# Kernel tuning notes

Hardware: AMD Instinct MI355X
Metric: run time of the kernel (lower is better)

The kernel has to match this reference:

```python
import jax, jax.numpy as jnp
import numpy as np

P = 7          # window size
HEADS = 8
DIM_HEAD = 32
INNER = HEADS * DIM_HEAD  # 256
DIM_IN = 256
DIM_OUT = 256
SCALE = DIM_HEAD ** -0.5


def _rel_index(p):
    i = np.array([[x, y] for x in range(p) for y in range(p)])  # (p*p, 2)
    d = i[None, :, :] - i[:, None, :]                            # (p*p, p*p, 2)
    return jnp.asarray(d + p - 1, dtype=jnp.int32)


def setup_inputs() -> dict:
    key = jax.random.key(0)
    ks = jax.random.split(key, 6)
    x = jax.random.normal(ks[0], (16, DIM_IN, 112, 112), dtype=jnp.float32)
    Wq = jax.random.normal(ks[1], (INNER, DIM_IN), dtype=jnp.float32) * 0.02
    Wkv = jax.random.normal(ks[2], (2 * INNER, DIM_IN), dtype=jnp.float32) * 0.02
    Wo = jax.random.normal(ks[3], (DIM_OUT, INNER), dtype=jnp.float32) * 0.02
    bo = jax.random.normal(ks[4], (DIM_OUT,), dtype=jnp.float32) * 0.02
    pos_embedding = jax.random.normal(ks[5], (2 * P - 1, 2 * P - 1), dtype=jnp.float32) * 0.02
    rel_index = _rel_index(P)
    return {"x": x, "Wq": Wq, "Wkv": Wkv, "Wo": Wo, "bo": bo,
            "pos_embedding": pos_embedding, "rel_index": rel_index}


def _local_attention(x, Wq, Wkv, Wo, bo, pos_embedding, rel_index):
    b, c, h, w = x.shape
    n1, n2 = h // P, w // P
    n = P * P
    # relative position bias (p^2, p^2)
    bias = pos_embedding[rel_index[:, :, 0], rel_index[:, :, 1]]
    # window partition: (b, c, n1, P, n2, P) -> (b*n1*n2, c, P*P)
    xw = x.reshape(b, c, n1, P, n2, P).transpose(0, 2, 4, 1, 3, 5)
    xw = xw.reshape(b * n1 * n2, c, n)
    # 1x1 conv projections as channel GEMMs
    q = jnp.einsum('oc,bcn->bon', Wq, xw)       # (B', INNER, n)
    kv = jnp.einsum('oc,bcn->bon', Wkv, xw)     # (B', 2*INNER, n)
    k, v = kv[:, :INNER], kv[:, INNER:]

    def to_heads(t):  # (B', H*d, n) -> (B', H, n, d)
        Bp = t.shape[0]
        return t.reshape(Bp, HEADS, DIM_HEAD, n).transpose(0, 1, 3, 2)

    q, k, v = to_heads(q), to_heads(k), to_heads(v)
    dots = jnp.einsum('bhid,bhjd->bhij', q, k) * SCALE + bias
    attn = jax.nn.softmax(dots, axis=-1)
    out = jnp.einsum('bhij,bhjd->bhid', attn, v)          # (B', H, n, d)
    out = out.transpose(0, 1, 3, 2).reshape(-1, INNER, n)  # (B', H*d, n)
    out = jnp.einsum('oc,bcn->bon', Wo, out) + bo[None, :, None]
    # window merge back to (b, c_out, h, w)
    out = out.reshape(b, n1, n2, DIM_OUT, P, P).transpose(0, 3, 1, 4, 2, 5)
    out = out.reshape(b, DIM_OUT, h, w)
    return out, attn


def reference(x, Wq, Wkv, Wo, bo, pos_embedding, rel_index):
    return _local_attention(x, Wq, Wkv, Wo, bo, pos_embedding, rel_index)
```

## Files before the change

### kernel.cpp

```cpp
#include <hip/hip_runtime.h>
#include <hip/hip_bf16.h>

typedef __bf16 bf16x8 __attribute__((ext_vector_type(8)));
typedef __bf16 bf16x4 __attribute__((ext_vector_type(4)));
typedef float  f32x4  __attribute__((ext_vector_type(4)));
typedef float  f32x16 __attribute__((ext_vector_type(16)));

#define NPOS 49
#define NHEADS 8
#define SCALE_F 0.17677669529663687f

#define SLICE_B   16896
#define QK_ROW_B  264
#define VS_OFF    8192
#define VS_ROW_B  136
#define XWT_PITCH 264
#define AOT_PITCH 264
#define BIAS_OFF  67584
#define BO_OFF    77188
#define LDS_BYTES 78212

static __device__ __forceinline__ f32x16 zero16() {
  f32x16 z;
#pragma unroll
  for (int i = 0; i < 16; ++i) z[i] = 0.f;
  return z;
}

__global__ void prep_kernel(const float* __restrict__ Wq, const float* __restrict__ Wkv,
                            const float* __restrict__ Wo, const float* __restrict__ pos,
                            const int* __restrict__ rel, __bf16* __restrict__ wqkv,
                            __bf16* __restrict__ wo, float* __restrict__ bias) {
  int idx = blockIdx.x * 256 + threadIdx.x;
  if (idx < 256 * 256) wqkv[idx] = (__bf16)Wq[idx];
  if (idx < 512 * 256) wqkv[256 * 256 + idx] = (__bf16)Wkv[idx];
  if (idx < 256 * 256) wo[idx] = (__bf16)Wo[idx];
  if (idx < 49 * 49) bias[idx] = pos[rel[idx * 2] * 13 + rel[idx * 2 + 1]];
}

template <int MODE>
__global__ __launch_bounds__(256, 2) void attn_kernel(
    const float* __restrict__ x, const __bf16* __restrict__ wqkv,
    const __bf16* __restrict__ wo, const float* __restrict__ bias_g,
    const float* __restrict__ bo_g, float* __restrict__ outg,
    float* __restrict__ attng, __bf16* __restrict__ aoT_g) {
  extern __shared__ char smem[];
  __bf16* xwT = (__bf16*)smem;
  __bf16* aoT = (__bf16*)smem;
  float* bias_s = (float*)(smem + BIAS_OFF);
  float* bo_s   = (float*)(smem + BO_OFF);

  const int tid = threadIdx.x;
  const int bid = blockIdx.x;
  const int work = (bid & 7) * 512 + (bid >> 3);
  const int b  = work >> 8;
  const int i1 = (work >> 4) & 15;
  const int i2 = work & 15;
  const int r0 = i1 * 7, c0 = i2 * 7;
  const int wave = tid >> 6, lane = tid & 63;
  const int l31 = lane & 31, g2 = lane >> 5;
  const int c16 = lane & 15, g4 = lane >> 4;
  char* slice = smem + wave * SLICE_B;

  {
    const int n = tid & 63, cb = tid >> 6;
    const int np = (n < NPOS) ? n : 0;
    const float zf = (n < NPOS) ? 1.f : 0.f;
    const int pr = np / 7, pc = np - pr * 7;
    const float* xg = x + (size_t)b * 256 * 12544 + (size_t)(r0 + pr) * 112 + (c0 + pc);
    float tmp[64];
#pragma unroll
    for (int it = 0; it < 64; ++it)
      tmp[it] = xg[(size_t)(it * 4 + cb) * 12544];
#pragma unroll
    for (int it = 0; it < 64; ++it)
      xwT[n * XWT_PITCH + it * 4 + cb] = (__bf16)(tmp[it] * zf);
    const float4* bg4 = (const float4*)bias_g;
    for (int i = tid; i < 600; i += 256) ((float4*)bias_s)[i] = bg4[i];
    if (tid == 0) bias_s[2400] = bias_g[2400];
    if constexpr (MODE == 0) bo_s[tid] = bo_g[tid];
  }
  __syncthreads();

  bf16x8 Bf0[16], Bf1[16];
  {
    const __bf16* Bp = xwT + l31 * XWT_PITCH + g2 * 8;
#pragma unroll
    for (int ks = 0; ks < 16; ++ks) {
      Bf0[ks] = *(const bf16x8*)(Bp + ks * 16);
      Bf1[ks] = *(const bf16x8*)(Bp + 32 * XWT_PITCH + ks * 16);
    }
  }
  __syncthreads();

  char* vsb = slice + VS_OFF;
  {
    const __bf16* Ap0 = wqkv + (size_t)(512 + 64 * wave + l31) * 256 + g2 * 8;
    const __bf16* Ap1 = Ap0 + 32 * 256;
    f32x16 a00 = zero16(), a01 = zero16(), a10 = zero16(), a11 = zero16();
    __builtin_amdgcn_s_setprio(1);
#pragma unroll
    for (int ks = 0; ks < 16; ++ks) {
      bf16x8 A0 = *(const bf16x8*)(Ap0 + ks * 16);
      bf16x8 A1 = *(const bf16x8*)(Ap1 + ks * 16);
      a00 = __builtin_amdgcn_mfma_f32_32x32x16_bf16(A0, Bf0[ks], a00, 0, 0, 0);
      a01 = __builtin_amdgcn_mfma_f32_32x32x16_bf16(A0, Bf1[ks], a01, 0, 0, 0);
      a10 = __builtin_amdgcn_mfma_f32_32x32x16_bf16(A1, Bf0[ks], a10, 0, 0, 0);
      a11 = __builtin_amdgcn_mfma_f32_32x32x16_bf16(A1, Bf1[ks], a11, 0, 0, 0);
    }
    __builtin_amdgcn_s_setprio(0);
#pragma unroll
    for (int rg = 0; rg < 16; ++rg) {
      const int dd = (rg & 3) + 8 * (rg >> 2) + 4 * g2;
      *(__bf16*)(vsb + dd * VS_ROW_B + l31 * 2)              = (__bf16)a00[rg];
      *(__bf16*)(vsb + dd * VS_ROW_B + 64 + l31 * 2)         = (__bf16)a01[rg];
      *(__bf16*)(vsb + (32 + dd) * VS_ROW_B + l31 * 2)       = (__bf16)a10[rg];
      *(__bf16*)(vsb + (32 + dd) * VS_ROW_B + 64 + l31 * 2)  = (__bf16)a11[rg];
    }
  }
  bf16x8 vf[2][2][2];
#pragma unroll
  for (int hh = 0; hh < 2; ++hh)
#pragma unroll
    for (int nt = 0; nt < 2; ++nt)
#pragma unroll
      for (int ks = 0; ks < 2; ++ks)
        vf[hh][nt][ks] = *(const bf16x8*)(vsb + (hh * 32 + nt * 16 + c16) * VS_ROW_B + ks * 64 + g4 * 16);
  asm volatile("s_waitcnt lgkmcnt(0)" ::: "memory");
  __builtin_amdgcn_sched_barrier(0x20);

#pragma unroll
  for (int qk = 0; qk < 2; ++qk) {
    const int rowbase = qk * 256 + 64 * wave;
    const int koff = qk * 64;
    const __bf16* Ap0 = wqkv + (size_t)(rowbase + l31) * 256 + g2 * 8;
    const __bf16* Ap1 = Ap0 + 32 * 256;
    f32x16 a00 = zero16(), a01 = zero16(), a10 = zero16(), a11 = zero16();
    __builtin_amdgcn_s_setprio(1);
#pragma unroll
    for (int ks = 0; ks < 16; ++ks) {
      bf16x8 A0 = *(const bf16x8*)(Ap0 + ks * 16);
      bf16x8 A1 = *(const bf16x8*)(Ap1 + ks * 16);
      a00 = __builtin_amdgcn_mfma_f32_32x32x16_bf16(A0, Bf0[ks], a00, 0, 0, 0);
      a01 = __builtin_amdgcn_mfma_f32_32x32x16_bf16(A0, Bf1[ks], a01, 0, 0, 0);
      a10 = __builtin_amdgcn_mfma_f32_32x32x16_bf16(A1, Bf0[ks], a10, 0, 0, 0);
      a11 = __builtin_amdgcn_mfma_f32_32x32x16_bf16(A1, Bf1[ks], a11, 0, 0, 0);
    }
    __builtin_amdgcn_s_setprio(0);
#define STORE_QK(ACC, P_, NT)                                                  \
    {                                                                          \
      const int n_ = (NT) * 32 + l31;                                          \
      _Pragma("unroll") for (int rb = 0; rb < 4; ++rb) {                       \
        const int ddb = koff + (P_) * 32 + rb * 8 + g2 * 4;                    \
        bf16x4 v4;                                                             \
        v4[0] = (__bf16)ACC[rb * 4 + 0]; v4[1] = (__bf16)ACC[rb * 4 + 1];      \
        v4[2] = (__bf16)ACC[rb * 4 + 2]; v4[3] = (__bf16)ACC[rb * 4 + 3];      \
        *(bf16x4*)(slice + n_ * QK_ROW_B + ddb * 2) = v4;                      \
      }                                                                        \
    }
    STORE_QK(a00, 0, 0)
    STORE_QK(a01, 0, 1)
    STORE_QK(a10, 1, 0)
    STORE_QK(a11, 1, 1)
  }
  bf16x8 qf[2][4], kf[2][4];
#pragma unroll
  for (int hh = 0; hh < 2; ++hh)
#pragma unroll
    for (int t = 0; t < 4; ++t) {
      qf[hh][t] = *(const bf16x8*)(slice + (t * 16 + c16) * QK_ROW_B + hh * 64 + g4 * 16);
      kf[hh][t] = *(const bf16x8*)(slice + (t * 16 + c16) * QK_ROW_B + 128 + hh * 64 + g4 * 16);
    }
  asm volatile("s_waitcnt lgkmcnt(0)" ::: "memory");
  __builtin_amdgcn_sched_barrier(0x20);

  f32x4 pacc[2][4][2];
  char* Pb0 = slice;
  char* Pb1 = slice + 8192;
  {
    const f32x4 z4 = {0.f, 0.f, 0.f, 0.f};
    f32x4 dacc[2][4][4];
    __builtin_amdgcn_s_setprio(1);
#pragma unroll
    for (int hh = 0; hh < 2; ++hh)
#pragma unroll
      for (int mt = 0; mt < 4; ++mt)
#pragma unroll
        for (int nt = 0; nt < 4; ++nt)
          dacc[hh][mt][nt] = __builtin_amdgcn_mfma_f32_16x16x32_bf16(qf[hh][mt], kf[hh][nt], z4, 0, 0, 0);
    __builtin_amdgcn_s_setprio(0);

    const int h0 = wave * 2;
#pragma unroll
    for (int mt = 0; mt < 4; ++mt) {
#pragma unroll
      for (int r = 0; r < 4; ++r) {
        const int i = mt * 16 + g4 * 4 + r;
        float p0[4], p1[4], s0 = 0.f, s1 = 0.f;
#pragma unroll
        for (int nt = 0; nt < 4; ++nt) {
          const int j = nt * 16 + c16;
          float v0 = dacc[0][mt][nt][r] * SCALE_F;
          float v1 = dacc[1][mt][nt][r] * SCALE_F;
          if (j < NPOS) {
            if (i < NPOS) { const float bb = bias_s[i * 49 + j]; v0 += bb; v1 += bb; }
          } else {
            v0 = -1e30f; v1 = -1e30f;
          }
          p0[nt] = __expf(v0); s0 += p0[nt];
          p1[nt] = __expf(v1); s1 += p1[nt];
        }
        s0 += __shfl_xor(s0, 1); s1 += __shfl_xor(s1, 1);
        s0 += __shfl_xor(s0, 2); s1 += __shfl_xor(s1, 2);
        s0 += __shfl_xor(s0, 4); s1 += __shfl_xor(s1, 4);
        s0 += __shfl_xor(s0, 8); s1 += __shfl_xor(s1, 8);
        const float inv0 = 1.f / s0, inv1 = 1.f / s1;
        if (i < NPOS) {
          float* ap0 = attng + ((size_t)(work * NHEADS + h0) * 49 + i) * 49;
          float* ap1 = ap0 + 49 * 49;
#pragma unroll
          for (int nt = 0; nt < 4; ++nt) {
            const int j = nt * 16 + c16;
            if (j < NPOS) { ap0[j] = p0[nt] * inv0; ap1[j] = p1[nt] * inv1; }
          }
        }
#pragma unroll
        for (int nt = 0; nt < 4; ++nt) {
          const int j = nt * 16 + c16;
          *(__bf16*)(Pb0 + i * 128 + 16 * ((j >> 3) ^ (i & 7)) + 2 * (j & 7)) = (__bf16)(p0[nt] * inv0);
          *(__bf16*)(Pb1 + i * 128 + 16 * ((j >> 3) ^ (i & 7)) + 2 * (j & 7)) = (__bf16)(p1[nt] * inv1);
        }
      }
    }

    __builtin_amdgcn_s_setprio(1);
#pragma unroll
    for (int hh = 0; hh < 2; ++hh) {
      char* Pb = hh ? Pb1 : Pb0;
#pragma unroll
      for (int mt = 0; mt < 4; ++mt) {
        const int i = mt * 16 + c16;
        bf16x8 pa0 = *(const bf16x8*)(Pb + i * 128 + 16 * ((0 + g4) ^ (i & 7)));
        bf16x8 pa1 = *(const bf16x8*)(Pb + i * 128 + 16 * ((4 + g4) ^ (i & 7)));
#pragma unroll
        for (int nt = 0; nt < 2; ++nt) {
          f32x4 acc = {0.f, 0.f, 0.f, 0.f};
          acc = __builtin_amdgcn_mfma_f32_16x16x32_bf16(pa0, vf[hh][nt][0], acc, 0, 0, 0);
          acc = __builtin_amdgcn_mfma_f32_16x16x32_bf16(pa1, vf[hh][nt][1], acc, 0, 0, 0);
          pacc[hh][mt][nt] = acc;
        }
      }
    }
    __builtin_amdgcn_s_setprio(0);
  }

  if constexpr (MODE == 1) {
    __bf16* ag = aoT_g + (size_t)work * 12544;
#pragma unroll
    for (int hh = 0; hh < 2; ++hh) {
      const int h = wave * 2 + hh;
#pragma unroll
      for (int mt = 0; mt < 4; ++mt)
#pragma unroll
        for (int e = 0; e < 4; ++e) {
          const int pos = mt * 16 + g4 * 4 + e;
          if (pos < NPOS) {
            ag[pos * 256 + h * 32 + c16]      = (__bf16)pacc[hh][mt][0][e];
            ag[pos * 256 + h * 32 + 16 + c16] = (__bf16)pacc[hh][mt][1][e];
          }
        }
    }
  } else {
    __syncthreads();
#pragma unroll
    for (int hh = 0; hh < 2; ++hh) {
      const int h = wave * 2 + hh;
#pragma unroll
      for (int mt = 0; mt < 4; ++mt)
#pragma unroll
        for (int nt = 0; nt < 2; ++nt)
#pragma unroll
          for (int e = 0; e < 4; ++e) {
            const int i = mt * 16 + g4 * 4 + e;
            const int cc = h * 32 + nt * 16 + c16;
            aoT[i * AOT_PITCH + cc] = (__bf16)pacc[hh][mt][nt][e];
          }
    }
    __syncthreads();
    {
      bf16x8 Cf0[16], Cf1[16];
      const __bf16* Bp = aoT + l31 * AOT_PITCH + g2 * 8;
#pragma unroll
      for (int ks = 0; ks < 16; ++ks) {
        Cf0[ks] = *(const bf16x8*)(Bp + ks * 16);
        Cf1[ks] = *(const bf16x8*)(Bp + 32 * AOT_PITCH + ks * 16);
      }
      const __bf16* Ap0 = wo + (size_t)(wave * 64 + l31) * 256 + g2 * 8;
      const __bf16* Ap1 = Ap0 + 32 * 256;
      f32x16 a00 = zero16(), a01 = zero16(), a10 = zero16(), a11 = zero16();
      __builtin_amdgcn_s_setprio(1);
#pragma unroll
      for (int ks = 0; ks < 16; ++ks) {
        bf16x8 A0 = *(const bf16x8*)(Ap0 + ks * 16);
        bf16x8 A1 = *(const bf16x8*)(Ap1 + ks * 16);
        a00 = __builtin_amdgcn_mfma_f32_32x32x16_bf16(A0, Cf0[ks], a00, 0, 0, 0);
        a01 = __builtin_amdgcn_mfma_f32_32x32x16_bf16(A0, Cf1[ks], a01, 0, 0, 0);
        a10 = __builtin_amdgcn_mfma_f32_32x32x16_bf16(A1, Cf0[ks], a10, 0, 0, 0);
        a11 = __builtin_amdgcn_mfma_f32_32x32x16_bf16(A1, Cf1[ks], a11, 0, 0, 0);
      }
      __builtin_amdgcn_s_setprio(0);
      float* og = outg + (size_t)b * 256 * 12544;
#define STORE_OUT(ACC, MT, NT)                                                    \
      {                                                                           \
        const int n_ = (NT) * 32 + l31;                                           \
        if (n_ < NPOS) {                                                          \
          const int pr_ = n_ / 7, pc_ = n_ - pr_ * 7;                             \
          float* orow = og + (size_t)(r0 + pr_) * 112 + (c0 + pc_);               \
          _Pragma("unroll") for (int rg = 0; rg < 16; ++rg) {                     \
            const int o2 = wave * 64 + (MT) * 32 + (rg & 3) + 8 * (rg >> 2) + 4 * g2; \
            orow[(size_t)o2 * 12544] = ACC[rg] + bo_s[o2];                        \
          }                                                                       \
        }                                                                         \
      }
      STORE_OUT(a00, 0, 0)
      STORE_OUT(a01, 0, 1)
      STORE_OUT(a10, 1, 0)
      STORE_OUT(a11, 1, 1)
    }
  }
}

__global__ __launch_bounds__(256, 2) void oproj_kernel(
    const __bf16* __restrict__ aoT_g, const __bf16* __restrict__ wo,
    const float* __restrict__ bo_g, float* __restrict__ outg) {
  __shared__ __bf16 aoB[112 * 264];
  __shared__ float bo_s[256];
  const int tid = threadIdx.x;
  const int bid = blockIdx.x;
  const int work = (bid & 7) * 224 + (bid >> 3);
  const int pr = work % 7;
  const int g  = work / 7;
  const int i1 = g & 15, b = g >> 4;
  const int wave = tid >> 6, lane = tid & 63;
  const int c16 = lane & 15, g4 = lane >> 4;

  {
    const int rr = tid >> 5, coff = (tid & 31) * 8;
#pragma unroll
    for (int it = 0; it < 14; ++it) {
      const int gr = it * 8 + rr;
      const int i2 = gr / 7, pc = gr - i2 * 7;
      const size_t src = ((size_t)((b * 256 + i1 * 16 + i2) * 49 + pr * 7 + pc)) * 256 + coff;
      *(bf16x8*)(aoB + gr * 264 + coff) = *(const bf16x8*)(aoT_g + src);
    }
    bo_s[tid] = bo_g[tid];
  }
  __syncthreads();

  const int oc0 = wave * 64;
  f32x4 acc[4][7];
#pragma unroll
  for (int mt = 0; mt < 4; ++mt)
#pragma unroll
    for (int nt = 0; nt < 7; ++nt) acc[mt][nt] = f32x4{0.f, 0.f, 0.f, 0.f};
#pragma unroll
  for (int kk = 0; kk < 8; ++kk) {
    bf16x8 Af[4], Bf[7];
#pragma unroll
    for (int mt = 0; mt < 4; ++mt)
      Af[mt] = *(const bf16x8*)(wo + (size_t)(oc0 + mt * 16 + c16) * 256 + kk * 32 + g4 * 8);
#pragma unroll
    for (int nt = 0; nt < 7; ++nt)
      Bf[nt] = *(const bf16x8*)(aoB + (nt * 16 + c16) * 264 + kk * 32 + g4 * 8);
    __builtin_amdgcn_s_setprio(1);
#pragma unroll
    for (int mt = 0; mt < 4; ++mt)
#pragma unroll
      for (int nt = 0; nt < 7; ++nt)
        acc[mt][nt] = __builtin_amdgcn_mfma_f32_16x16x32_bf16(Af[mt], Bf[nt], acc[mt][nt], 0, 0, 0);
    __builtin_amdgcn_s_setprio(0);
  }
  float* orow = outg + (size_t)b * 256 * 12544 + (size_t)(i1 * 7 + pr) * 112;
#pragma unroll
  for (int mt = 0; mt < 4; ++mt)
#pragma unroll
    for (int e = 0; e < 4; ++e) {
      const int oc = oc0 + mt * 16 + g4 * 4 + e;
      const float bb = bo_s[oc];
#pragma unroll
      for (int nt = 0; nt < 7; ++nt)
        orow[(size_t)oc * 12544 + nt * 16 + c16] = acc[mt][nt][e] + bb;
    }
}

extern "C" void kernel_launch(void* const* d_in, const int* in_sizes, int n_in,
                              void* d_out, int out_size, void* d_ws, size_t ws_size,
                              hipStream_t stream) {
  const float* x   = (const float*)d_in[0];
  const float* Wq  = (const float*)d_in[1];
  const float* Wkv = (const float*)d_in[2];
  const float* Wo  = (const float*)d_in[3];
  const float* bo  = (const float*)d_in[4];
  const float* pos = (const float*)d_in[5];
  const int*   rel = (const int*)d_in[6];

  float* outg  = (float*)d_out;
  float* attng = outg + (size_t)16 * 256 * 112 * 112;

  __bf16* wqkv = (__bf16*)d_ws;
  __bf16* wo   = wqkv + 768 * 256;
  float*  bias = (float*)(wo + 256 * 256);

  size_t base = 768 * 256 * 2 + 256 * 256 * 2 + 2401 * 4;
  base = (base + 255) & ~(size_t)255;
  const size_t ao_bytes = (size_t)4096 * 12544 * 2;
  const bool split = (ws_size >= base + ao_bytes);
  __bf16* aoT_g = (__bf16*)((char*)d_ws + base);

  hipFuncSetAttribute((const void*)attn_kernel<0>,
                      hipFuncAttributeMaxDynamicSharedMemorySize, LDS_BYTES);
  hipFuncSetAttribute((const void*)attn_kernel<1>,
                      hipFuncAttributeMaxDynamicSharedMemorySize, LDS_BYTES);

  prep_kernel<<<dim3(512), dim3(256), 0, stream>>>(Wq, Wkv, Wo, pos, rel, wqkv, wo, bias);
  if (split) {
    attn_kernel<1><<<dim3(4096), dim3(256), LDS_BYTES, stream>>>(
        x, wqkv, wo, bias, bo, outg, attng, aoT_g);
    oproj_kernel<<<dim3(1792), dim3(256), 0, stream>>>(aoT_g, wo, bo, outg);
  } else {
    attn_kernel<0><<<dim3(4096), dim3(256), LDS_BYTES, stream>>>(
        x, wqkv, wo, bias, bo, outg, attng, nullptr);
  }
}
```

Baseline: 487.2 us.

## Split fused attention kernel into separate QKV projection and attention kernels

Adds a three-stage path: a QKV projection kernel that writes Q, K and transposed V to workspace in bf16, an attention kernel (one head per wave, two blocks per window) computing softmax and P·V, and the existing output projection kernel. The aim is to raise occupancy and shrink per-kernel LDS and register pressure compared with the monolithic attention kernel. In exchange it adds a global-memory round trip for Q/K/V, about 650 MB of extra traffic, and needs a larger workspace, falling back to the old path otherwise.

```diff
diff --git a/kernel.cpp b/kernel.cpp
--- a/kernel.cpp
+++ b/kernel.cpp
@@ -20,6 +20,10 @@
 #define BO_OFF    77188
 #define LDS_BYTES 78212
 
+#define XW2_PITCH 268
+#define QKV_LDS   (64 * XW2_PITCH * 2)
+#define ATT_LDS   (4 * 8192)
+
 static __device__ __forceinline__ f32x16 zero16() {
   f32x16 z;
 #pragma unroll
@@ -36,6 +40,197 @@
   if (idx < 512 * 256) wqkv[256 * 256 + idx] = (__bf16)Wkv[idx];
   if (idx < 256 * 256) wo[idx] = (__bf16)Wo[idx];
   if (idx < 49 * 49) bias[idx] = pos[rel[idx * 2] * 13 + rel[idx * 2 + 1]];
+}
+
+__global__ __launch_bounds__(256, 4) void qkv_kernel(
+    const float* __restrict__ x, const __bf16* __restrict__ wqkv,
+    __bf16* __restrict__ qg, __bf16* __restrict__ kg, __bf16* __restrict__ vtg) {
+  extern __shared__ char smem[];
+  __bf16* xwT = (__bf16*)smem;
+
+  const int tid = threadIdx.x;
+  const int bid = blockIdx.x;
+  const int work = (bid & 7) * 512 + (bid >> 3);
+  const int b  = work >> 8;
+  const int i1 = (work >> 4) & 15;
+  const int i2 = work & 15;
+  const int r0 = i1 * 7, c0 = i2 * 7;
+  const int wave = tid >> 6, lane = tid & 63;
+  const int l31 = lane & 31, g2 = lane >> 5;
+
+  {
+    const int n = tid & 63, cb = tid >> 6;
+    const int np = (n < NPOS) ? n : 0;
+    const float zf = (n < NPOS) ? 1.f : 0.f;
+    const int pr = np / 7, pc = np - pr * 7;
+    const float* xg = x + (size_t)b * 256 * 12544 + (size_t)(r0 + pr) * 112 + (c0 + pc);
+    float tmp[64];
+#pragma unroll
+    for (int it = 0; it < 64; ++it)
+      tmp[it] = xg[(size_t)(it * 4 + cb) * 12544];
+#pragma unroll
+    for (int it = 0; it < 64; ++it)
+      xwT[n * XW2_PITCH + it * 4 + cb] = (__bf16)(tmp[it] * zf);
+  }
+  __syncthreads();
+
+  const size_t hb = (size_t)work * 8;
+
+#pragma unroll 1
+  for (int p = 3 * wave; p < 3 * wave + 3; ++p) {
+    const __bf16* Ap0 = wqkv + (size_t)(64 * p + l31) * 256 + g2 * 8;
+    const __bf16* Ap1 = Ap0 + 32 * 256;
+    const __bf16* Bp  = xwT + l31 * XW2_PITCH + g2 * 8;
+    f32x16 a00 = zero16(), a01 = zero16(), a10 = zero16(), a11 = zero16();
+    __builtin_amdgcn_s_setprio(1);
+#pragma unroll
+    for (int ks = 0; ks < 16; ++ks) {
+      bf16x8 B0 = *(const bf16x8*)(Bp + ks * 16);
+      bf16x8 B1 = *(const bf16x8*)(Bp + 32 * XW2_PITCH + ks * 16);
+      bf16x8 A0 = *(const bf16x8*)(Ap0 + ks * 16);
+      bf16x8 A1 = *(const bf16x8*)(Ap1 + ks * 16);
+      a00 = __builtin_amdgcn_mfma_f32_32x32x16_bf16(A0, B0, a00, 0, 0, 0);
+      a01 = __builtin_amdgcn_mfma_f32_32x32x16_bf16(A0, B1, a01, 0, 0, 0);
+      a10 = __builtin_amdgcn_mfma_f32_32x32x16_bf16(A1, B0, a10, 0, 0, 0);
+      a11 = __builtin_amdgcn_mfma_f32_32x32x16_bf16(A1, B1, a11, 0, 0, 0);
+    }
+    __builtin_amdgcn_s_setprio(0);
+#define QKV_STORE(ACC, S, NT)                                                  \
+    {                                                                          \
+      const int sec = (S) >> 3, h = (S) & 7;                                   \
+      const int n_ = (NT) * 32 + l31;                                          \
+      if (sec < 2) {                                                           \
+        if (n_ < NPOS) {                                                       \
+          __bf16* bp = (sec ? kg : qg) + (hb + h) * 1568 + n_ * 32;            \
+          _Pragma("unroll") for (int rb = 0; rb < 4; ++rb) {                   \
+            bf16x4 v4;                                                         \
+            v4[0] = (__bf16)ACC[rb * 4 + 0]; v4[1] = (__bf16)ACC[rb * 4 + 1];  \
+            v4[2] = (__bf16)ACC[rb * 4 + 2]; v4[3] = (__bf16)ACC[rb * 4 + 3];  \
+            *(bf16x4*)(bp + 8 * rb + 4 * g2) = v4;                             \
+          }                                                                    \
+        }                                                                      \
+      } else {                                                                 \
+        __bf16* vp = vtg + (hb + h) * 2048 + n_;                               \
+        _Pragma("unroll") for (int rg = 0; rg < 16; ++rg) {                    \
+          const int dd = (rg & 3) + 8 * (rg >> 2) + 4 * g2;                    \
+          vp[dd * 64] = (__bf16)ACC[rg];                                       \
+        }                                                                      \
+      }                                                                        \
+    }
+    QKV_STORE(a00, 2 * p, 0)
+    QKV_STORE(a01, 2 * p, 1)
+    QKV_STORE(a10, 2 * p + 1, 0)
+    QKV_STORE(a11, 2 * p + 1, 1)
+  }
+}
+
+__global__ __launch_bounds__(256, 3) void att_kernel(
+    const __bf16* __restrict__ qg, const __bf16* __restrict__ kg,
+    const __bf16* __restrict__ vtg, const float* __restrict__ bias_g,
+    float* __restrict__ attng, __bf16* __restrict__ aoT_g) {
+  extern __shared__ char smem[];
+  const int tid = threadIdx.x;
+  const int bid = blockIdx.x;
+  const int work = (bid & 7) * 1024 + (bid >> 3);
+  const int win  = work >> 1;
+  const int wave = tid >> 6, lane = tid & 63;
+  const int head = (work & 1) * 4 + wave;
+  const int c16 = lane & 15, g4 = lane >> 4;
+  char* Pb = smem + wave * 8192;
+
+  const size_t hidx = (size_t)win * 8 + head;
+  const __bf16* qb = qg + hidx * 1568;
+  const __bf16* kb = kg + hidx * 1568;
+  const __bf16* vb = vtg + hidx * 2048;
+
+  bf16x8 qf[4], kf[4];
+#pragma unroll
+  for (int t = 0; t < 4; ++t) {
+    int rr = t * 16 + c16; rr = rr > 48 ? 48 : rr;
+    qf[t] = *(const bf16x8*)(qb + rr * 32 + g4 * 8);
+    kf[t] = *(const bf16x8*)(kb + rr * 32 + g4 * 8);
+  }
+  bf16x8 vf[2][2];
+#pragma unroll
+  for (int nt = 0; nt < 2; ++nt)
+#pragma unroll
+    for (int ks = 0; ks < 2; ++ks)
+      vf[nt][ks] = *(const bf16x8*)(vb + (nt * 16 + c16) * 64 + ks * 32 + g4 * 8);
+
+  f32x4 dacc[4][4];
+  const f32x4 z4 = {0.f, 0.f, 0.f, 0.f};
+  __builtin_amdgcn_s_setprio(1);
+#pragma unroll
+  for (int mt = 0; mt < 4; ++mt)
+#pragma unroll
+    for (int nt = 0; nt < 4; ++nt)
+      dacc[mt][nt] = __builtin_amdgcn_mfma_f32_16x16x32_bf16(qf[mt], kf[nt], z4, 0, 0, 0);
+  __builtin_amdgcn_s_setprio(0);
+
+#pragma unroll
+  for (int mt = 0; mt < 4; ++mt) {
+#pragma unroll
+    for (int r = 0; r < 4; ++r) {
+      const int i = mt * 16 + g4 * 4 + r;
+      float p[4], s = 0.f;
+#pragma unroll
+      for (int nt = 0; nt < 4; ++nt) {
+        const int j = nt * 16 + c16;
+        float val = dacc[mt][nt][r] * SCALE_F;
+        if (j < NPOS) {
+          if (i < NPOS) val += bias_g[i * 49 + j];
+        } else {
+          val = -1e30f;
+        }
+        p[nt] = __expf(val); s += p[nt];
+      }
+      s += __shfl_xor(s, 1); s += __shfl_xor(s, 2);
+      s += __shfl_xor(s, 4); s += __shfl_xor(s, 8);
+      const float inv = 1.f / s;
+      if (i < NPOS) {
+        float* ap = attng + ((size_t)(win * NHEADS + head) * 49 + i) * 49;
+#pragma unroll
+        for (int nt = 0; nt < 4; ++nt) {
+          const int j = nt * 16 + c16;
+          if (j < NPOS) ap[j] = p[nt] * inv;
+        }
+      }
+#pragma unroll
+      for (int nt = 0; nt < 4; ++nt) {
+        const int j = nt * 16 + c16;
+        *(__bf16*)(Pb + i * 128 + 16 * ((j >> 3) ^ (i & 7)) + 2 * (j & 7)) = (__bf16)(p[nt] * inv);
+      }
+    }
+  }
+
+  f32x4 pacc[4][2];
+  __builtin_amdgcn_s_setprio(1);
+#pragma unroll
+  for (int mt = 0; mt < 4; ++mt) {
+    const int i = mt * 16 + c16;
+    bf16x8 pa0 = *(const bf16x8*)(Pb + i * 128 + 16 * ((0 + g4) ^ (i & 7)));
+    bf16x8 pa1 = *(const bf16x8*)(Pb + i * 128 + 16 * ((4 + g4) ^ (i & 7)));
+#pragma unroll
+    for (int nt = 0; nt < 2; ++nt) {
+      f32x4 acc = {0.f, 0.f, 0.f, 0.f};
+      acc = __builtin_amdgcn_mfma_f32_16x16x32_bf16(pa0, vf[nt][0], acc, 0, 0, 0);
+      acc = __builtin_amdgcn_mfma_f32_16x16x32_bf16(pa1, vf[nt][1], acc, 0, 0, 0);
+      pacc[mt][nt] = acc;
+    }
+  }
+  __builtin_amdgcn_s_setprio(0);
+
+  __bf16* ag = aoT_g + (size_t)win * 12544;
+#pragma unroll
+  for (int mt = 0; mt < 4; ++mt)
+#pragma unroll
+    for (int e = 0; e < 4; ++e) {
+      const int pos = mt * 16 + g4 * 4 + e;
+      if (pos < NPOS) {
+        ag[pos * 256 + head * 32 + c16]      = (__bf16)pacc[mt][0][e];
+        ag[pos * 256 + head * 32 + 16 + c16] = (__bf16)pacc[mt][1][e];
+      }
+    }
 }
 
 template <int MODE>
@@ -414,16 +609,33 @@
   size_t base = 768 * 256 * 2 + 256 * 256 * 2 + 2401 * 4;
   base = (base + 255) & ~(size_t)255;
   const size_t ao_bytes = (size_t)4096 * 12544 * 2;
-  const bool split = (ws_size >= base + ao_bytes);
+  const size_t qk_bytes = (size_t)4096 * 8 * 3136;
+  const size_t vt_bytes = (size_t)4096 * 8 * 4096;
+  const size_t q_off = base + ao_bytes;
+  const size_t k_off = q_off + qk_bytes;
+  const size_t v_off = k_off + qk_bytes;
+  const size_t full  = v_off + vt_bytes;
+
   __bf16* aoT_g = (__bf16*)((char*)d_ws + base);
+  __bf16* qg    = (__bf16*)((char*)d_ws + q_off);
+  __bf16* kg    = (__bf16*)((char*)d_ws + k_off);
+  __bf16* vtg   = (__bf16*)((char*)d_ws + v_off);
 
   hipFuncSetAttribute((const void*)attn_kernel<0>,
                       hipFuncAttributeMaxDynamicSharedMemorySize, LDS_BYTES);
   hipFuncSetAttribute((const void*)attn_kernel<1>,
                       hipFuncAttributeMaxDynamicSharedMemorySize, LDS_BYTES);
+  hipFuncSetAttribute((const void*)qkv_kernel,
+                      hipFuncAttributeMaxDynamicSharedMemorySize, QKV_LDS);
+  hipFuncSetAttribute((const void*)att_kernel,
+                      hipFuncAttributeMaxDynamicSharedMemorySize, ATT_LDS);
 
   prep_kernel<<<dim3(512), dim3(256), 0, stream>>>(Wq, Wkv, Wo, pos, rel, wqkv, wo, bias);
-  if (split) {
+  if (ws_size >= full) {
+    qkv_kernel<<<dim3(4096), dim3(256), QKV_LDS, stream>>>(x, wqkv, qg, kg, vtg);
+    att_kernel<<<dim3(8192), dim3(256), ATT_LDS, stream>>>(qg, kg, vtg, bias, attng, aoT_g);
+    oproj_kernel<<<dim3(1792), dim3(256), 0, stream>>>(aoT_g, wo, bo, outg);
+  } else if (ws_size >= base + ao_bytes) {
     attn_kernel<1><<<dim3(4096), dim3(256), LDS_BYTES, stream>>>(
         x, wqkv, wo, bias, bo, outg, attng, aoT_g);
     oproj_kernel<<<dim3(1792), dim3(256), 0, stream>>>(aoT_g, wo, bo, outg);
```

Result: slower. 605.1 us (+24.2%).

## Pre-swizzle weights into MFMA fragment order and vectorize window gather of x

Applied to the files above, without the earlier changes.

The prep kernel now writes extra copies of Wqkv and Wo in bf16, laid out so that each lane's MFMA A-fragment sits contiguously and a wave's loads coalesce into one 1KB chunk. The goal is to cut the strided 16-byte weight loads in the QKV and output-projection GEMMs. The x window gather also changes from per-element strided loads (one channel per loop step) to row-wise vector loads of 7 contiguous floats, plus explicit zeroing of the padding rows. This costs a larger workspace and extra prep work, and LDS stores during the transpose are now scattered.

```diff
diff --git a/kernel.cpp b/kernel.cpp
--- a/kernel.cpp
+++ b/kernel.cpp
@@ -5,6 +5,8 @@
 typedef __bf16 bf16x4 __attribute__((ext_vector_type(4)));
 typedef float  f32x4  __attribute__((ext_vector_type(4)));
 typedef float  f32x16 __attribute__((ext_vector_type(16)));
+typedef float  f32x4a __attribute__((ext_vector_type(4))) __attribute__((aligned(4)));
+typedef float  f32x2a __attribute__((ext_vector_type(2))) __attribute__((aligned(4)));
 
 #define NPOS 49
 #define NHEADS 8
@@ -30,17 +32,30 @@
 __global__ void prep_kernel(const float* __restrict__ Wq, const float* __restrict__ Wkv,
                             const float* __restrict__ Wo, const float* __restrict__ pos,
                             const int* __restrict__ rel, __bf16* __restrict__ wqkv,
-                            __bf16* __restrict__ wo, float* __restrict__ bias) {
-  int idx = blockIdx.x * 256 + threadIdx.x;
-  if (idx < 256 * 256) wqkv[idx] = (__bf16)Wq[idx];
-  if (idx < 512 * 256) wqkv[256 * 256 + idx] = (__bf16)Wkv[idx];
-  if (idx < 256 * 256) wo[idx] = (__bf16)Wo[idx];
+                            __bf16* __restrict__ wo, float* __restrict__ bias,
+                            __bf16* __restrict__ wqkvP, __bf16* __restrict__ woP) {
+  const int idx = blockIdx.x * 256 + threadIdx.x;
+  const int row = idx >> 8, col = idx & 255;
+  const float wv = (row < 256) ? Wq[idx] : Wkv[idx - 65536];
+  wqkv[idx] = (__bf16)wv;
+  {
+    const int s = row >> 5, l31 = row & 31;
+    const int ks = col >> 4, g2 = (col >> 3) & 1, e = col & 7;
+    wqkvP[((size_t)((s * 16 + ks) * 64 + g2 * 32 + l31)) * 8 + e] = (__bf16)wv;
+  }
+  if (idx < 65536) {
+    const float w = Wo[idx];
+    wo[idx] = (__bf16)w;
+    const int t = row >> 4, c16 = row & 15;
+    const int kk = col >> 5, g4 = (col >> 3) & 3, e = col & 7;
+    woP[((size_t)((t * 8 + kk) * 64 + g4 * 16 + c16)) * 8 + e] = (__bf16)w;
+  }
   if (idx < 49 * 49) bias[idx] = pos[rel[idx * 2] * 13 + rel[idx * 2 + 1]];
 }
 
 template <int MODE>
 __global__ __launch_bounds__(256, 2) void attn_kernel(
-    const float* __restrict__ x, const __bf16* __restrict__ wqkv,
+    const float* __restrict__ x, const __bf16* __restrict__ wqkvP,
     const __bf16* __restrict__ wo, const float* __restrict__ bias_g,
     const float* __restrict__ bo_g, float* __restrict__ outg,
     float* __restrict__ attng, __bf16* __restrict__ aoT_g) {
@@ -63,18 +78,39 @@
   char* slice = smem + wave * SLICE_B;
 
   {
-    const int n = tid & 63, cb = tid >> 6;
-    const int np = (n < NPOS) ? n : 0;
-    const float zf = (n < NPOS) ? 1.f : 0.f;
-    const int pr = np / 7, pc = np - pr * 7;
-    const float* xg = x + (size_t)b * 256 * 12544 + (size_t)(r0 + pr) * 112 + (c0 + pc);
-    float tmp[64];
-#pragma unroll
-    for (int it = 0; it < 64; ++it)
-      tmp[it] = xg[(size_t)(it * 4 + cb) * 12544];
-#pragma unroll
-    for (int it = 0; it < 64; ++it)
-      xwT[n * XWT_PITCH + it * 4 + cb] = (__bf16)(tmp[it] * zf);
+    bf16x8 z8;
+#pragma unroll
+    for (int j = 0; j < 8; ++j) z8[j] = (__bf16)0.f;
+    for (int i = tid; i < 480; i += 256) {
+      const int row = 49 + (i >> 5);
+      const int col = (i & 31) * 8;
+      *(bf16x8*)(xwT + row * XWT_PITCH + col) = z8;
+    }
+    f32x4a b4[7]; f32x2a b2[7]; float b1[7];
+    int chv[7], rowv[7];
+    const float* xb = x + (size_t)b * 256 * 12544;
+#pragma unroll
+    for (int k = 0; k < 7; ++k) {
+      const int p = k * 256 + tid;
+      const int ch = p / 7;
+      const int row = p - ch * 7;
+      chv[k] = ch; rowv[k] = row;
+      const float* xr = xb + (size_t)ch * 12544 + (size_t)(r0 + row) * 112 + c0;
+      b4[k] = *(const f32x4a*)xr;
+      b2[k] = *(const f32x2a*)(xr + 4);
+      b1[k] = xr[6];
+    }
+#pragma unroll
+    for (int k = 0; k < 7; ++k) {
+      __bf16* dst = xwT + (rowv[k] * 7) * XWT_PITCH + chv[k];
+      dst[0 * XWT_PITCH] = (__bf16)b4[k][0];
+      dst[1 * XWT_PITCH] = (__bf16)b4[k][1];
+      dst[2 * XWT_PITCH] = (__bf16)b4[k][2];
+      dst[3 * XWT_PITCH] = (__bf16)b4[k][3];
+      dst[4 * XWT_PITCH] = (__bf16)b2[k][0];
+      dst[5 * XWT_PITCH] = (__bf16)b2[k][1];
+      dst[6 * XWT_PITCH] = (__bf16)b1[k];
+    }
     const float4* bg4 = (const float4*)bias_g;
     for (int i = tid; i < 600; i += 256) ((float4*)bias_s)[i] = bg4[i];
     if (tid == 0) bias_s[2400] = bias_g[2400];
@@ -95,14 +131,14 @@
 
   char* vsb = slice + VS_OFF;
   {
-    const __bf16* Ap0 = wqkv + (size_t)(512 + 64 * wave + l31) * 256 + g2 * 8;
-    const __bf16* Ap1 = Ap0 + 32 * 256;
+    const __bf16* A0p = wqkvP + (size_t)(16 + 2 * wave) * 8192 + lane * 8;
+    const __bf16* A1p = A0p + 8192;
     f32x16 a00 = zero16(), a01 = zero16(), a10 = zero16(), a11 = zero16();
     __builtin_amdgcn_s_setprio(1);
 #pragma unroll
     for (int ks = 0; ks < 16; ++ks) {
-      bf16x8 A0 = *(const bf16x8*)(Ap0 + ks * 16);
-      bf16x8 A1 = *(const bf16x8*)(Ap1 + ks * 16);
+      bf16x8 A0 = *(const bf16x8*)(A0p + ks * 512);
+      bf16x8 A1 = *(const bf16x8*)(A1p + ks * 512);
       a00 = __builtin_amdgcn_mfma_f32_32x32x16_bf16(A0, Bf0[ks], a00, 0, 0, 0);
       a01 = __builtin_amdgcn_mfma_f32_32x32x16_bf16(A0, Bf1[ks], a01, 0, 0, 0);
       a10 = __builtin_amdgcn_mfma_f32_32x32x16_bf16(A1, Bf0[ks], a10, 0, 0, 0);
@@ -131,16 +167,15 @@
 
 #pragma unroll
   for (int qk = 0; qk < 2; ++qk) {
-    const int rowbase = qk * 256 + 64 * wave;
     const int koff = qk * 64;
-    const __bf16* Ap0 = wqkv + (size_t)(rowbase + l31) * 256 + g2 * 8;
-    const __bf16* Ap1 = Ap0 + 32 * 256;
+    const __bf16* A0p = wqkvP + (size_t)(2 * wave + qk * 8) * 8192 + lane * 8;
+    const __bf16* A1p = A0p + 8192;
     f32x16 a00 = zero16(), a01 = zero16(), a10 = zero16(), a11 = zero16();
     __builtin_amdgcn_s_setprio(1);
 #pragma unroll
     for (int ks = 0; ks < 16; ++ks) {
-      bf16x8 A0 = *(const bf16x8*)(Ap0 + ks * 16);
-      bf16x8 A1 = *(const bf16x8*)(Ap1 + ks * 16);
+      bf16x8 A0 = *(const bf16x8*)(A0p + ks * 512);
+      bf16x8 A1 = *(const bf16x8*)(A1p + ks * 512);
       a00 = __builtin_amdgcn_mfma_f32_32x32x16_bf16(A0, Bf0[ks], a00, 0, 0, 0);
       a01 = __builtin_amdgcn_mfma_f32_32x32x16_bf16(A0, Bf1[ks], a01, 0, 0, 0);
       a10 = __builtin_amdgcn_mfma_f32_32x32x16_bf16(A1, Bf0[ks], a10, 0, 0, 0);
@@ -331,7 +366,7 @@
 }
 
 __global__ __launch_bounds__(256, 2) void oproj_kernel(
-    const __bf16* __restrict__ aoT_g, const __bf16* __restrict__ wo,
+    const __bf16* __restrict__ aoT_g, const __bf16* __restrict__ woP,
     const float* __restrict__ bo_g, float* __restrict__ outg) {
   __shared__ __bf16 aoB[112 * 264];
   __shared__ float bo_s[256];
@@ -358,6 +393,7 @@
   __syncthreads();
 
   const int oc0 = wave * 64;
+  const __bf16* Ap = woP + ((size_t)wave * 4 * 8) * 512 + lane * 8;
   f32x4 acc[4][7];
 #pragma unroll
   for (int mt = 0; mt < 4; ++mt)
@@ -368,7 +404,7 @@
     bf16x8 Af[4], Bf[7];
 #pragma unroll
     for (int mt = 0; mt < 4; ++mt)
-      Af[mt] = *(const bf16x8*)(wo + (size_t)(oc0 + mt * 16 + c16) * 256 + kk * 32 + g4 * 8);
+      Af[mt] = *(const bf16x8*)(Ap + (size_t)(mt * 8 + kk) * 512);
 #pragma unroll
     for (int nt = 0; nt < 7; ++nt)
       Bf[nt] = *(const bf16x8*)(aoB + (nt * 16 + c16) * 264 + kk * 32 + g4 * 8);
@@ -407,28 +443,30 @@
   float* outg  = (float*)d_out;
   float* attng = outg + (size_t)16 * 256 * 112 * 112;
 
-  __bf16* wqkv = (__bf16*)d_ws;
-  __bf16* wo   = wqkv + 768 * 256;
-  float*  bias = (float*)(wo + 256 * 256);
-
-  size_t base = 768 * 256 * 2 + 256 * 256 * 2 + 2401 * 4;
+  __bf16* wqkv  = (__bf16*)d_ws;
+  __bf16* wo    = (__bf16*)((char*)d_ws + 393216);
+  float*  bias  = (float*)((char*)d_ws + 393216 + 131072);
+  __bf16* wqkvP = (__bf16*)((char*)d_ws + 393216 + 131072 + 9728);
+  __bf16* woP   = (__bf16*)((char*)d_ws + 393216 + 131072 + 9728 + 393216);
+  size_t base = 393216 + 131072 + 9728 + 393216 + 131072;
   base = (base + 255) & ~(size_t)255;
   const size_t ao_bytes = (size_t)4096 * 12544 * 2;
-  const bool split = (ws_size >= base + ao_bytes);
   __bf16* aoT_g = (__bf16*)((char*)d_ws + base);
+  (void)wqkv;
 
   hipFuncSetAttribute((const void*)attn_kernel<0>,
                       hipFuncAttributeMaxDynamicSharedMemorySize, LDS_BYTES);
   hipFuncSetAttribute((const void*)attn_kernel<1>,
                       hipFuncAttributeMaxDynamicSharedMemorySize, LDS_BYTES);
 
-  prep_kernel<<<dim3(512), dim3(256), 0, stream>>>(Wq, Wkv, Wo, pos, rel, wqkv, wo, bias);
-  if (split) {
+  prep_kernel<<<dim3(768), dim3(256), 0, stream>>>(Wq, Wkv, Wo, pos, rel, wqkv, wo, bias,
+                                                   wqkvP, woP);
+  if (ws_size >= base + ao_bytes) {
     attn_kernel<1><<<dim3(4096), dim3(256), LDS_BYTES, stream>>>(
-        x, wqkv, wo, bias, bo, outg, attng, aoT_g);
-    oproj_kernel<<<dim3(1792), dim3(256), 0, stream>>>(aoT_g, wo, bo, outg);
+        x, wqkvP, wo, bias, bo, outg, attng, aoT_g);
+    oproj_kernel<<<dim3(1792), dim3(256), 0, stream>>>(aoT_g, woP, bo, outg);
   } else {
     attn_kernel<0><<<dim3(4096), dim3(256), LDS_BYTES, stream>>>(
-        x, wqkv, wo, bias, bo, outg, attng, nullptr);
+        x, wqkvP, wo, bias, bo, outg, attng, nullptr);
   }
 }
```

Result: faster. 426.0 us (-12.6%).
